# Optimization experiments

Measured on AMD Instinct MI355X. Metric: run time of the kernel, lower is better.

Reference implementation:

```python
import jax, jax.numpy as jnp
import numpy as np

B, S, N = 16, 64, 4096
D = 64            # input_dim*seq_len == output_dim*graph_dim
FEAT = 64
E = 32768
HEADS = (3, 3, 1)
NEG_SLOPE = 0.2   # PyG GATConv default negative_slope


def _lin_init(key, fi, fo):
    k1, k2 = jax.random.split(key)
    s = 1.0 / np.sqrt(fi)
    return (jax.random.uniform(k1, (fi, fo), jnp.float32, -s, s),
            jax.random.uniform(k2, (fo,), jnp.float32, -s, s))


def setup_inputs() -> dict:
    key = jax.random.key(0)
    ks = jax.random.split(key, 32)
    inp = {}
    inp["inputs"] = jax.random.normal(ks[0], (B, S, N, 1), jnp.float32)
    inp["edge_index"] = jax.random.randint(ks[1], (2, E), 0, N, dtype=jnp.int32)
    inp["W_seq"], inp["b_seq"] = _lin_init(ks[2], D, D)
    inp["src_embed"] = jax.random.normal(ks[3], (N, FEAT), jnp.float32) * 0.1
    inp["tgt_embed"] = jax.random.normal(ks[4], (FEAT, N), jnp.float32) * 0.1
    for i, H in enumerate(HEADS):
        s = 1.0 / np.sqrt(D)
        inp[f"Wg{i}"] = jax.random.uniform(ks[5 + 5 * i], (D, H * D), jnp.float32, -s, s)
        inp[f"asrc{i}"] = jax.random.normal(ks[6 + 5 * i], (H, D), jnp.float32) * 0.1
        inp[f"adst{i}"] = jax.random.normal(ks[7 + 5 * i], (H, D), jnp.float32) * 0.1
        inp[f"bg{i}"] = jnp.zeros((D,), jnp.float32)
        inp[f"Wl{i}"], inp[f"bl{i}"] = _lin_init(ks[8 + 5 * i], D, D)
    inp["Wo"], inp["bo"] = _lin_init(ks[25], D, D)
    return inp


def _gat(x, src, dst, W, a_src, a_dst, b):
    # PyG GATConv, concat=False (mean over heads). x: [B,N,D] -> [B,N,D]
    H, C = a_src.shape
    xp = jnp.einsum('bnd,dhc->bnhc', x, W.reshape(D, H, C))       # [B,N,H,C]
    al_s = jnp.einsum('bnhc,hc->bnh', xp, a_src)
    al_d = jnp.einsum('bnhc,hc->bnh', xp, a_dst)
    e = jax.nn.leaky_relu(al_s[:, src] + al_d[:, dst], NEG_SLOPE)  # [B,Et,H]

    def per_graph(e_b, xj_b):
        m = jax.ops.segment_max(e_b, dst, num_segments=N)          # [N,H]
        w = jnp.exp(e_b - m[dst])
        z = jax.ops.segment_sum(w, dst, num_segments=N)
        alpha = w / z[dst]                                         # softmax per dst node
        return jax.ops.segment_sum(xj_b * alpha[..., None], dst, num_segments=N)

    out = jax.vmap(per_graph)(e, xp[:, src])                       # [B,N,H,C]
    return out.mean(axis=2) + b


def _forward(inputs, edge_index, W_seq, b_seq, src_embed, tgt_embed,
             Wg0, asrc0, adst0, bg0, Wl0, bl0,
             Wg1, asrc1, adst1, bg1, Wl1, bl1,
             Wg2, asrc2, adst2, bg2, Wl2, bl2, Wo, bo):
    loop = jnp.arange(N, dtype=edge_index.dtype)
    src = jnp.concatenate([edge_index[0], loop])   # PyG add_self_loops=True
    dst = jnp.concatenate([edge_index[1], loop])
    h = inputs.transpose(0, 2, 3, 1).reshape(B * N, D)
    h = h @ W_seq + b_seq + h                       # seq_linear residual
    A = jax.nn.softmax(jax.nn.relu(src_embed @ tgt_embed), axis=1)  # learned adjacency [N,N]
    gat_p = [(Wg0, asrc0, adst0, bg0), (Wg1, asrc1, adst1, bg1), (Wg2, asrc2, adst2, bg2)]
    lin_p = [(Wl0, bl0), (Wl1, bl1), (Wl2, bl2)]
    for i in range(3):
        hb = h.reshape(B, N, D)
        # layer-0 GAT output is computed but unused in the original code (dead); skip it
        h_cur = _gat(hb, src, dst, *gat_p[i]).reshape(B * N, D) if i > 0 else None
        adp = jnp.einsum('mn,bnd->bmd', A, hb)      # adaptive-graph matmul (dropout in eval = identity)
        adp = (adp @ lin_p[i][0] + lin_p[i][1]).reshape(B * N, D)
        g = jax.nn.sigmoid(adp)
        if i == 0:
            origin = h @ Wo + bo
            h = jnp.tanh(h) * g + origin * (1.0 - g)
        elif i == 1:
            h = jax.nn.leaky_relu(h_cur, 0.01) * g + h * (1.0 - g)
        else:
            h = jax.nn.relu(h_cur) * g + h * (1.0 - g)
    return h.reshape(B, N, 1, D)   # [batch, node_num, output_dim, graph_dim]


def reference(inputs, edge_index, W_seq, b_seq, src_embed, tgt_embed,
              Wg0, asrc0, adst0, bg0, Wl0, bl0,
              Wg1, asrc1, adst1, bg1, Wl1, bl1,
              Wg2, asrc2, adst2, bg2, Wl2, bl2, Wo, bo):
    return _forward(inputs, edge_index, W_seq, b_seq, src_embed, tgt_embed,
                    Wg0, asrc0, adst0, bg0, Wl0, bl0,
                    Wg1, asrc1, adst1, bg1, Wl1, bl1,
                    Wg2, asrc2, adst2, bg2, Wl2, bl2, Wo, bo)
```

## Files before the change

### kernel.cpp

```cpp
#include <hip/hip_runtime.h>
#include <stdint.h>

#define NB 16
#define NN 4096
#define DD 64
#define EE 32768
#define ETOT 36864
#define ROWS 65536
#define KSPLIT 2

typedef _Float16 f16;
typedef f16   half8 __attribute__((ext_vector_type(8)));
typedef f16   f16x8 __attribute__((ext_vector_type(8)));
typedef f16   f16x4 __attribute__((ext_vector_type(4)));
typedef float f32x4 __attribute__((ext_vector_type(4)));

__device__ __forceinline__ void gload16(const f16* g, f16* l) {
  __builtin_amdgcn_global_load_lds((const __attribute__((address_space(1))) void*)g,
                                   (__attribute__((address_space(3))) void*)l, 16, 0, 0);
}

__global__ __launch_bounds__(256) void k_zero2(int* a, int* b) {
  int i = blockIdx.x * 256 + threadIdx.x;
  if (i < NN) a[i] = 0;
  else if (i < 2 * NN) b[i - NN] = 0;
}

__global__ __launch_bounds__(256) void k_count(const int* __restrict__ ei, int* __restrict__ cnt) {
  int t = blockIdx.x * 256 + threadIdx.x;
  if (t >= ETOT) return;
  int d = (t < EE) ? ei[EE + t] : (t - EE);
  atomicAdd(&cnt[d], 1);
}

__global__ __launch_bounds__(256) void k_scan(const int* __restrict__ cnt, int* __restrict__ offs) {
  __shared__ int part[256];
  int t = threadIdx.x;
  int loc[16]; int s = 0;
  #pragma unroll
  for (int i = 0; i < 16; ++i) { int v = cnt[(t << 4) + i]; loc[i] = s; s += v; }
  part[t] = s;
  __syncthreads();
  int own = s;
  for (int d = 1; d < 256; d <<= 1) {
    int u = (t >= d) ? part[t - d] : 0;
    __syncthreads();
    part[t] += u;
    __syncthreads();
  }
  int base = part[t] - own;
  #pragma unroll
  for (int i = 0; i < 16; ++i) offs[(t << 4) + i] = base + loc[i];
}

__global__ __launch_bounds__(256) void k_fill(const int* __restrict__ ei, const int* __restrict__ offs,
                                              int* __restrict__ cur, int* __restrict__ esrc,
                                              int* __restrict__ edst) {
  int t = blockIdx.x * 256 + threadIdx.x;
  if (t >= ETOT) return;
  int s, d;
  if (t < EE) { s = ei[t]; d = ei[EE + t]; } else { s = d = t - EE; }
  int p = atomicAdd(&cur[d], 1);
  esrc[offs[d] + p] = s;
  edst[offs[d] + p] = d;
}

__global__ __launch_bounds__(256) void k_seq(const float* __restrict__ inp, const float* __restrict__ Wseq,
                                             const float* __restrict__ bseq, float* __restrict__ h) {
  __shared__ float X[64 * 68];
  int t = threadIdx.x;
  int b = blockIdx.x >> 6, n0 = (blockIdx.x & 63) << 6;
  #pragma unroll
  for (int i = 0; i < 16; ++i) {
    int idx = t + (i << 8);
    int s = idx >> 6, nl = idx & 63;
    X[nl * 68 + s] = inp[((size_t)((b << 6) + s) << 12) + n0 + nl];
  }
  __syncthreads();
  int c = t & 63, rg = t >> 6;
  float Wc[64];
  #pragma unroll
  for (int k = 0; k < 64; ++k) Wc[k] = Wseq[(k << 6) + c];
  float bc = bseq[c];
  for (int rr = 0; rr < 16; ++rr) {
    int r = (rg << 4) + rr;
    float a = bc + X[r * 68 + c];
    #pragma unroll
    for (int k4 = 0; k4 < 16; ++k4) {
      float4 x = *(const float4*)&X[r * 68 + (k4 << 2)];
      a = fmaf(x.x, Wc[4*k4+0], a); a = fmaf(x.y, Wc[4*k4+1], a);
      a = fmaf(x.z, Wc[4*k4+2], a); a = fmaf(x.w, Wc[4*k4+3], a);
    }
    h[((size_t)(b << 12) + n0 + r) * 64 + c] = a;
  }
}

__global__ __launch_bounds__(256) void k_adjmm(const f16* __restrict__ SEh, const f16* __restrict__ TEh,
                                               f16* __restrict__ A, float* __restrict__ Zpart) {
  __shared__ f16 Al[2][128 * 32];
  __shared__ f16 Bl[2][128 * 32];
  const int t = threadIdx.x, lane = t & 63, w = t >> 6;
  const int m0 = blockIdx.y << 7, j0 = blockIdx.x << 7;
  const int l15 = lane & 15, lhi = lane >> 4;
  const int wm = (w >> 1) << 6, wj = (w & 1) << 6;
  f32x4 acc[4][4] = {};
  const int c0 = (w << 6) + lane;
  const int row0 = c0 >> 2, ko0 = (c0 & 3) << 3;
  const int c1 = c0 + 256;
  const int row1 = c1 >> 2, ko1 = (c1 & 3) << 3;
  const f16* ga0 = SEh + (size_t)(m0 + row0) * 64 + ko0;
  const f16* ga1 = SEh + (size_t)(m0 + row1) * 64 + ko1;
  const f16* gb0 = TEh + (size_t)(j0 + row0) * 64 + ko0;
  const f16* gb1 = TEh + (size_t)(j0 + row1) * 64 + ko1;
  #pragma unroll
  for (int kt = 0; kt < 2; ++kt) {
    const int kof = kt << 5;
    gload16(ga0 + kof, Al[kt] + c0 * 8);
    gload16(ga1 + kof, Al[kt] + c1 * 8);
    gload16(gb0 + kof, Bl[kt] + c0 * 8);
    gload16(gb1 + kof, Bl[kt] + c1 * 8);
  }
  __syncthreads();
  #pragma unroll
  for (int kt = 0; kt < 2; ++kt) {
    half8 af[4], bf[4];
    #pragma unroll
    for (int i = 0; i < 4; ++i) {
      af[i] = *(const half8*)(Al[kt] + (wm + i * 16 + l15) * 32 + lhi * 8);
      bf[i] = *(const half8*)(Bl[kt] + (wj + i * 16 + l15) * 32 + lhi * 8);
    }
    #pragma unroll
    for (int mi = 0; mi < 4; ++mi)
      #pragma unroll
      for (int nj = 0; nj < 4; ++nj)
        acc[mi][nj] = __builtin_amdgcn_mfma_f32_16x16x32_f16(af[mi], bf[nj], acc[mi][nj], 0, 0, 0);
  }
  float rs[4][4];
  #pragma unroll
  for (int mi = 0; mi < 4; ++mi)
    #pragma unroll
    for (int r = 0; r < 4; ++r) rs[mi][r] = 0.f;
  #pragma unroll
  for (int mi = 0; mi < 4; ++mi)
    #pragma unroll
    for (int nj = 0; nj < 4; ++nj)
      #pragma unroll
      for (int r = 0; r < 4; ++r) {
        int row = m0 + wm + mi * 16 + lhi * 4 + r;
        int col = j0 + wj + nj * 16 + l15;
        float e = __expf(fmaxf(acc[mi][nj][r], 0.f));
        f16 eh = (f16)e;
        A[((size_t)row << 12) + col] = eh;
        rs[mi][r] += (float)eh;
      }
  #pragma unroll
  for (int mi = 0; mi < 4; ++mi)
    #pragma unroll
    for (int r = 0; r < 4; ++r) {
      float s = rs[mi][r];
      s += __shfl_xor(s, 1); s += __shfl_xor(s, 2);
      s += __shfl_xor(s, 4); s += __shfl_xor(s, 8);
      rs[mi][r] = s;
    }
  if (l15 == 0) {
    int p = (blockIdx.x << 1) + (w & 1);
    #pragma unroll
    for (int mi = 0; mi < 4; ++mi)
      #pragma unroll
      for (int r = 0; r < 4; ++r)
        Zpart[((size_t)p << 12) + m0 + wm + mi * 16 + lhi * 4 + r] = rs[mi][r];
  }
}

__global__ __launch_bounds__(256) void k_rowz(const float* __restrict__ Zpart, float* __restrict__ rowZ) {
  int row = blockIdx.x * 256 + threadIdx.x;
  float s = 0.f;
  #pragma unroll 8
  for (int p = 0; p < 64; ++p) s += Zpart[((size_t)p << 12) + row];
  rowZ[row] = 1.f / s;
}

#define NKT 32
__global__ __launch_bounds__(512) void k_gemm8(const f16* __restrict__ A, const f16* __restrict__ BT,
                                               f16* __restrict__ Cout) {
  extern __shared__ f16 smem[];
  const int t = threadIdx.x, lane = t & 63, wid = t >> 6;
  const int wr = wid >> 1, wc = wid & 1;
  const int l15 = lane & 15, lhi = lane >> 4;
  const int h7 = l15 & 7;
  const int wgid = blockIdx.x;
  const int nid = (wgid & 7) * 32 + (wgid >> 3);
  const int z = nid >> 7, rem = nid & 127;
  const int m0 = (rem >> 3) << 8;
  const int j0 = (rem & 7) << 7;
  const size_t kbase = (size_t)z << 11;
  f16* __restrict__ Cz = Cout + ((size_t)z << 22);

  const f16* gA[4]; int lA[4];
  #pragma unroll
  for (int i = 0; i < 4; ++i) {
    int s = t + (i << 9), row = s >> 3, sl = (s & 7) ^ (row & 7);
    gA[i] = A + (size_t)(m0 + row) * 4096 + kbase + sl * 8;
    lA[i] = s * 8;
  }
  const f16* gB[2]; int lB[2];
  #pragma unroll
  for (int i = 0; i < 2; ++i) {
    int s = t + (i << 9), row = s >> 3, sl = (s & 7) ^ (row & 7);
    gB[i] = BT + (size_t)(j0 + row) * 4096 + kbase + sl * 8;
    lB[i] = 16384 + s * 8;
  }
  #define SA(buf, kt, i) gload16(gA[i] + (kt) * 64, smem + (buf) * 24576 + lA[i])
  #define SB(buf, kt, i) gload16(gB[i] + (kt) * 64, smem + (buf) * 24576 + lB[i])

  const int rbase = wr << 6;
  const int cbase = wc << 6;
  f32x4 acc[4][4] = {};

  #pragma unroll
  for (int i = 0; i < 4; ++i) SA(0, 0, i);
  #pragma unroll
  for (int i = 0; i < 2; ++i) SB(0, 0, i);
  #pragma unroll
  for (int i = 0; i < 4; ++i) SA(1, 1, i);
  #pragma unroll
  for (int i = 0; i < 2; ++i) SB(1, 1, i);
  asm volatile("s_waitcnt vmcnt(6)" ::: "memory");
  __builtin_amdgcn_sched_barrier(0);
  __builtin_amdgcn_s_barrier();
  __builtin_amdgcn_sched_barrier(0);

  int b0 = 0, b1 = 1, b2 = 2;
  for (int kt = 0; kt < NKT; ++kt) {
    const f16* Ab = smem + b0 * 24576;
    const f16* Bb = Ab + 16384;
    const bool pf = (kt + 2 < NKT);
    {
      half8 af[4], bf[4];
      #pragma unroll
      for (int mi = 0; mi < 4; ++mi) {
        int row = rbase + mi * 16 + l15;
        af[mi] = *(const half8*)(Ab + row * 64 + (lhi ^ h7) * 8);
      }
      #pragma unroll
      for (int nj = 0; nj < 4; ++nj) {
        int row = cbase + nj * 16 + l15;
        bf[nj] = *(const half8*)(Bb + row * 64 + (lhi ^ h7) * 8);
      }
      if (pf) { SA(b2, kt + 2, 0); SA(b2, kt + 2, 1); SA(b2, kt + 2, 2); }
      __builtin_amdgcn_s_setprio(1);
      #pragma unroll
      for (int mi = 0; mi < 4; ++mi)
        #pragma unroll
        for (int nj = 0; nj < 4; ++nj)
          acc[mi][nj] = __builtin_amdgcn_mfma_f32_16x16x32_f16(af[mi], bf[nj], acc[mi][nj], 0, 0, 0);
      __builtin_amdgcn_s_setprio(0);
    }
    __builtin_amdgcn_s_barrier();
    __builtin_amdgcn_sched_barrier(0);
    {
      half8 af[4], bf[4];
      #pragma unroll
      for (int mi = 0; mi < 4; ++mi) {
        int row = rbase + mi * 16 + l15;
        af[mi] = *(const half8*)(Ab + row * 64 + ((4 + lhi) ^ h7) * 8);
      }
      #pragma unroll
      for (int nj = 0; nj < 4; ++nj) {
        int row = cbase + nj * 16 + l15;
        bf[nj] = *(const half8*)(Bb + row * 64 + ((4 + lhi) ^ h7) * 8);
      }
      if (pf) { SA(b2, kt + 2, 3); SB(b2, kt + 2, 0); SB(b2, kt + 2, 1); }
      __builtin_amdgcn_s_setprio(1);
      #pragma unroll
      for (int mi = 0; mi < 4; ++mi)
        #pragma unroll
        for (int nj = 0; nj < 4; ++nj)
          acc[mi][nj] = __builtin_amdgcn_mfma_f32_16x16x32_f16(af[mi], bf[nj], acc[mi][nj], 0, 0, 0);
      __builtin_amdgcn_s_setprio(0);
    }
    if (kt < NKT - 2)       asm volatile("s_waitcnt vmcnt(6)" ::: "memory");
    else if (kt == NKT - 2) asm volatile("s_waitcnt vmcnt(0)" ::: "memory");
    __builtin_amdgcn_sched_barrier(0);
    __builtin_amdgcn_s_barrier();
    __builtin_amdgcn_sched_barrier(0);
    int tb = b0; b0 = b1; b1 = b2; b2 = tb;
  }
  #undef SA
  #undef SB
  #pragma unroll
  for (int mi = 0; mi < 4; ++mi)
    #pragma unroll
    for (int nj = 0; nj < 4; ++nj)
      #pragma unroll
      for (int r = 0; r < 4; ++r) {
        int row = m0 + rbase + mi * 16 + (lhi << 2) + r;
        int col = j0 + cbase + nj * 16 + l15;
        Cz[(size_t)row * 1024 + col] = (f16)acc[mi][nj][r];
      }
}

template<int H, int NP>
__device__ __forceinline__ void wprep_body(const float* __restrict__ Wg, const float* __restrict__ asrc,
                                           const float* __restrict__ adst, const float* __restrict__ Wl,
                                           f16* __restrict__ Wgh, int bid, int t) {
  const int WL0 = H * 64 + 16;
  for (int i = bid * 256 + t; i < NP * 64; i += 16 * 256) {
    int j = i >> 6, k = i & 63;
    float v;
    if (j < H * 64) {
      v = Wg[(size_t)k * (H * 64) + j];
    } else if (j < H * 64 + 2 * H) {
      int cc = j - H * 64, hh = cc >> 1;
      const float* a = ((cc & 1) ? adst : asrc) + (hh << 6);
      const float* wrow = Wg + (size_t)k * (H * 64) + (hh << 6);
      float s = 0.f;
      #pragma unroll 16
      for (int c = 0; c < 64; ++c) s = fmaf(wrow[c], a[c], s);
      v = s;
    } else if (j >= WL0 && j < WL0 + 64) {
      v = Wl[(k << 6) + (j - WL0)];
    } else v = 0.f;
    Wgh[(size_t)j * 64 + k] = (f16)v;
  }
}

__global__ __launch_bounds__(256) void k_allprep(
    const float* __restrict__ Wg1, const float* __restrict__ as1, const float* __restrict__ ad1,
    const float* __restrict__ Wl1, f16* __restrict__ Wgh1,
    const float* __restrict__ Wg2, const float* __restrict__ as2, const float* __restrict__ ad2,
    const float* __restrict__ Wl2, f16* __restrict__ Wgh2,
    const float* __restrict__ Wl0, const float* __restrict__ Wo, f16* __restrict__ W0h,
    const float* __restrict__ SE, const float* __restrict__ TE,
    f16* __restrict__ SEh, f16* __restrict__ TEh) {
  __shared__ float X[64 * 65];
  int bid = blockIdx.x, t = threadIdx.x;
  if (bid < 16) { wprep_body<3, 272>(Wg1, as1, ad1, Wl1, Wgh1, bid, t); return; }
  if (bid < 32) { wprep_body<1, 144>(Wg2, as2, ad2, Wl2, Wgh2, bid - 16, t); return; }
  if (bid < 40) {
    for (int i = (bid - 32) * 256 + t; i < 128 * 64; i += 8 * 256) {
      int j = i >> 6, k = i & 63;
      float v = (j < 64) ? Wl0[(k << 6) + j] : Wo[(k << 6) + (j - 64)];
      W0h[(size_t)j * 64 + k] = (f16)v;
    }
    return;
  }
  if (bid < 296) {
    int i = ((bid - 40) * 256 + t) * 4;
    float4 v = *(const float4*)(SE + i);
    f16 o[4] = {(f16)v.x, (f16)v.y, (f16)v.z, (f16)v.w};
    *(uint64_t*)(SEh + i) = *(uint64_t*)o;
    return;
  }
  int j0 = (bid - 296) << 6;
  #pragma unroll
  for (int i = 0; i < 16; ++i) {
    int idx = t + (i << 8);
    int k = idx >> 6, jl = idx & 63;
    X[jl * 65 + k] = TE[((size_t)k << 12) + j0 + jl];
  }
  __syncthreads();
  int jl = t >> 2, kg = t & 3;
  f16 o[16];
  #pragma unroll
  for (int i = 0; i < 16; ++i) o[i] = (f16)X[jl * 65 + (kg << 4) + i];
  f16* dst = TEh + ((size_t)(j0 + jl) << 6) + (kg << 4);
  *(uint64_t*)(dst + 0) = *(uint64_t*)(o + 0);
  *(uint64_t*)(dst + 4) = *(uint64_t*)(o + 4);
  *(uint64_t*)(dst + 8) = *(uint64_t*)(o + 8);
  *(uint64_t*)(dst + 12) = *(uint64_t*)(o + 12);
}

template<int H, int NP>
__global__ __launch_bounds__(256) void k_xpmm(const float* __restrict__ h, const f16* __restrict__ Wgh,
                                              f16* __restrict__ xp, float* __restrict__ als,
                                              float* __restrict__ ald, f16* __restrict__ HWlT) {
  const int WL0 = H * 64 + 16, JW0 = WL0 / 16, NT = NP / 16;
  __shared__ f16 Ah[64 * 72];
  __shared__ f16 Bh[NP * 72];
  __shared__ f16 stage[64 * 72];
  const int t = threadIdx.x, lane = t & 63, w = t >> 6;
  const size_t r0 = (size_t)blockIdx.x * 64;
  const int b = (int)(r0 >> 12), n0 = (int)(r0 & 4095);
  #pragma unroll
  for (int i = 0; i < 4; ++i) {
    int idx = t + (i << 8);
    int row = idx >> 4, k4 = (idx & 15) << 2;
    float4 v = *(const float4*)&h[(r0 + row) * 64 + k4];
    f16 o[4] = {(f16)v.x, (f16)v.y, (f16)v.z, (f16)v.w};
    *(uint64_t*)&Ah[row * 72 + k4] = *(uint64_t*)o;
  }
  for (int i = t; i < NP * 16; i += 256) {
    int row = i >> 4, k4 = (i & 15) << 2;
    *(uint64_t*)&Bh[row * 72 + k4] = *(const uint64_t*)&Wgh[(size_t)row * 64 + k4];
  }
  __syncthreads();
  const int l15 = lane & 15, lhi = lane >> 4;
  f32x4 acc[NT] = {};
  #pragma unroll
  for (int kk = 0; kk < 2; ++kk) {
    half8 af = *(const half8*)&Ah[(w * 16 + l15) * 72 + kk * 32 + lhi * 8];
    #pragma unroll
    for (int j = 0; j < NT; ++j) {
      half8 bf = *(const half8*)&Bh[(j * 16 + l15) * 72 + kk * 32 + lhi * 8];
      acc[j] = __builtin_amdgcn_mfma_f32_16x16x32_f16(af, bf, acc[j], 0, 0, 0);
    }
  }
  const int rl = w * 16 + lhi * 4;
  #pragma unroll
  for (int j = 0; j < NT; ++j) {
    int col = j * 16 + l15;
    if (j * 16 + 15 < H * 64) {
      #pragma unroll
      for (int r = 0; r < 4; ++r) {
        if (H == 3) xp[(r0 + rl + r) * 256 + ((col & 63) << 2) + (col >> 6)] = (f16)acc[j][r];
        else        xp[(r0 + rl + r) * 64 + col] = (f16)acc[j][r];
      }
    } else if (j < JW0) {
      int cc = col - H * 64;
      if (cc >= 0 && cc < 2 * H) {
        int hh = cc >> 1;
        #pragma unroll
        for (int r = 0; r < 4; ++r) {
          if (cc & 1) ald[(r0 + rl + r) * H + hh] = acc[j][r];
          else        als[(r0 + rl + r) * H + hh] = acc[j][r];
        }
      }
    } else {
      int e = col - WL0;
      f16 o[4] = {(f16)acc[j][0], (f16)acc[j][1], (f16)acc[j][2], (f16)acc[j][3]};
      *(uint64_t*)&stage[e * 72 + rl] = *(uint64_t*)o;
    }
  }
  __syncthreads();
  {
    int e = t >> 2, seg = (t & 3) << 4;
    float4 v0 = *(const float4*)&stage[e * 72 + seg];
    float4 v1 = *(const float4*)&stage[e * 72 + seg + 8];
    f16* dst = HWlT + (((size_t)((b << 6) + e)) << 12) + n0 + seg;
    *(float4*)dst = v0;
    *(float4*)(dst + 8) = v1;
  }
}

__global__ __launch_bounds__(256) void k_prep0(const float* __restrict__ h, const f16* __restrict__ W0h,
                                               f16* __restrict__ HWlT, f16* __restrict__ orig) {
  __shared__ f16 Ah[64 * 72];
  __shared__ f16 Bh[128 * 72];
  __shared__ f16 stage[64 * 72];
  const int t = threadIdx.x, lane = t & 63, w = t >> 6;
  const size_t r0 = (size_t)blockIdx.x * 64;
  const int b = (int)(r0 >> 12), n0 = (int)(r0 & 4095);
  #pragma unroll
  for (int i = 0; i < 4; ++i) {
    int idx = t + (i << 8);
    int row = idx >> 4, k4 = (idx & 15) << 2;
    float4 v = *(const float4*)&h[(r0 + row) * 64 + k4];
    f16 o[4] = {(f16)v.x, (f16)v.y, (f16)v.z, (f16)v.w};
    *(uint64_t*)&Ah[row * 72 + k4] = *(uint64_t*)o;
  }
  for (int i = t; i < 128 * 16; i += 256) {
    int row = i >> 4, k4 = (i & 15) << 2;
    *(uint64_t*)&Bh[row * 72 + k4] = *(const uint64_t*)&W0h[(size_t)row * 64 + k4];
  }
  __syncthreads();
  const int l15 = lane & 15, lhi = lane >> 4;
  f32x4 acc[8] = {};
  #pragma unroll
  for (int kk = 0; kk < 2; ++kk) {
    half8 af = *(const half8*)&Ah[(w * 16 + l15) * 72 + kk * 32 + lhi * 8];
    #pragma unroll
    for (int j = 0; j < 8; ++j) {
      half8 bf = *(const half8*)&Bh[(j * 16 + l15) * 72 + kk * 32 + lhi * 8];
      acc[j] = __builtin_amdgcn_mfma_f32_16x16x32_f16(af, bf, acc[j], 0, 0, 0);
    }
  }
  const int rl = w * 16 + lhi * 4;
  #pragma unroll
  for (int j = 0; j < 8; ++j) {
    int col = j * 16 + l15;
    if (j < 4) {
      f16 o[4] = {(f16)acc[j][0], (f16)acc[j][1], (f16)acc[j][2], (f16)acc[j][3]};
      *(uint64_t*)&stage[col * 72 + rl] = *(uint64_t*)o;
    } else {
      #pragma unroll
      for (int r = 0; r < 4; ++r)
        orig[(r0 + rl + r) * 64 + (col - 64)] = (f16)acc[j][r];
    }
  }
  __syncthreads();
  {
    int e = t >> 2, seg = (t & 3) << 4;
    float4 v0 = *(const float4*)&stage[e * 72 + seg];
    float4 v1 = *(const float4*)&stage[e * 72 + seg + 8];
    f16* dst = HWlT + (((size_t)((b << 6) + e)) << 12) + n0 + seg;
    *(float4*)dst = v0;
    *(float4*)(dst + 8) = v1;
  }
}

template<int H>
__global__ __launch_bounds__(256) void k_maxals(const float* __restrict__ als, float* __restrict__ Mals) {
  __shared__ float red[256];
  int b = blockIdx.x, t = threadIdx.x;
  size_t rbase = (size_t)b << 12;
  for (int h = 0; h < H; ++h) {
    float m = -1e30f;
    for (int n = t; n < NN; n += 256) m = fmaxf(m, als[(rbase + n) * H + h]);
    red[t] = m;
    __syncthreads();
    for (int d = 128; d; d >>= 1) {
      if (t < d) red[t] = fmaxf(red[t], red[t + d]);
      __syncthreads();
    }
    if (t == 0) Mals[b * H + h] = red[0];
    __syncthreads();
  }
}

template<int H>
__global__ __launch_bounds__(256) void k_wts(const float* __restrict__ als, const float* __restrict__ ald,
                                             const float* __restrict__ Mals, const int* __restrict__ esrc,
                                             const int* __restrict__ edst, float* __restrict__ wts) {
  const int WST = (H == 3) ? 4 : 1;
  int t = threadIdx.x, lane = t & 63, w = t >> 6;
  int gw = blockIdx.x * 4 + w;
  int b = gw & 15;
  int p = ((gw >> 4) << 6) + lane;
  size_t rbase = (size_t)b << 12;
  int s = esrc[p], n = edst[p];
  float* dst = wts + ((size_t)b * ETOT + p) * WST;
  #pragma unroll
  for (int h = 0; h < H; ++h) {
    float ad = ald[(rbase + n) * H + h];
    float B = Mals[b * H + h] + ad;
    float T = B > 0.f ? B : 0.2f * B;
    float ev = als[(rbase + s) * H + h] + ad;
    ev = ev > 0.f ? ev : 0.2f * ev;
    dst[h] = __expf(ev - T);
  }
}

template<int H, int ACT>
__global__ __launch_bounds__(256) void k_aggc(const f16* __restrict__ xp, const float* __restrict__ wts,
                                              const int* __restrict__ offs, const int* __restrict__ cnt,
                                              const int* __restrict__ esrc, const float* __restrict__ bg,
                                              const float* __restrict__ h, const f16* __restrict__ gp,
                                              const float* __restrict__ rowZ, const float* __restrict__ bl,
                                              float* __restrict__ hout) {
  const int WST = (H == 3) ? 4 : 1;
  __shared__ float wbuf[4][64 * WST];
  __shared__ int   sbuf[4][64];
  int t = threadIdx.x, lane = t & 63, wv = t >> 6;
  int blk = blockIdx.x;
  int b = ((blk & 7) << 1) | ((blk >> 3) & 1);
  int n = ((blk >> 4) << 2) + wv;
  size_t rbase = (size_t)b << 12;
  int o = offs[n], c = cnt[n];
  const float* wsrc = wts + ((size_t)b * ETOT + o) * WST;
  float z[H], acc[H];
  #pragma unroll
  for (int hh = 0; hh < H; ++hh) { z[hh] = 0.f; acc[hh] = 0.f; }
  for (int e0 = 0; e0 < c; e0 += 64) {
    int ce = min(64, c - e0);
    if (lane < ce) {
      sbuf[wv][lane] = esrc[o + e0 + lane];
      if (H == 3) *(float4*)&wbuf[wv][lane * 4] = *(const float4*)&wsrc[(size_t)(e0 + lane) * 4];
      else        wbuf[wv][lane] = wsrc[e0 + lane];
    }
    #pragma unroll 4
    for (int e = 0; e < ce; ++e) {
      int s = sbuf[wv][e];
      if (H == 3) {
        float4 w4 = *(const float4*)&wbuf[wv][e * 4];
        f16x4 q = *(const f16x4*)(xp + (((size_t)(rbase + s)) << 8) + (lane << 2));
        z[0] += w4.x; acc[0] = fmaf(w4.x, (float)q[0], acc[0]);
        z[1] += w4.y; acc[1] = fmaf(w4.y, (float)q[1], acc[1]);
        z[2] += w4.z; acc[2] = fmaf(w4.z, (float)q[2], acc[2]);
      } else {
        float wv_ = wbuf[wv][e];
        float xv = (float)xp[(((size_t)(rbase + s)) << 6) + lane];
        z[0] += wv_; acc[0] = fmaf(wv_, xv, acc[0]);
      }
    }
  }
  float r = 0.f;
  #pragma unroll
  for (int hh = 0; hh < H; ++hh) r += acc[hh] / z[hh];
  float cv = r * (1.f / H) + bg[lane];
  size_t ga = ((size_t)n << 10) + (b << 6) + lane;
  float zi = rowZ[n];
  float g0 = (float)gp[ga], g1 = (float)gp[ga + (size_t)(4096 * 1024)];
  float g = 1.f / (1.f + __expf(-((g0 + g1) * zi + bl[lane])));
  size_t ridx = ((rbase + n) << 6) + lane;
  float hv = h[ridx];
  float act = ACT ? fmaxf(cv, 0.f) : (cv > 0.f ? cv : 0.01f * cv);
  hout[ridx] = act * g + hv * (1.f - g);
}

__global__ __launch_bounds__(256) void k_comb0e(const float* __restrict__ h, const f16* __restrict__ gp,
                                                const float* __restrict__ rowZ, const f16* __restrict__ orig,
                                                const float* __restrict__ bl, const float* __restrict__ bo,
                                                float* __restrict__ hout) {
  for (size_t i4 = (size_t)blockIdx.x * 256 + threadIdx.x; i4 < (size_t)ROWS * 16; i4 += (size_t)2048 * 256) {
    size_t i = i4 * 4;
    int d = (int)(i & 63), n = (int)((i >> 6) & 4095), b = (int)(i >> 18);
    size_t ga = ((size_t)n << 10) + (b << 6) + d;
    float zi = rowZ[n];
    f16x4 g0 = *(const f16x4*)&gp[ga];
    f16x4 g1 = *(const f16x4*)&gp[ga + (size_t)(4096 * 1024)];
    f16x4 og = *(const f16x4*)&orig[i];
    float4 hv = *(const float4*)&h[i];
    float4 o;
    float* op = &o.x;
    const float* hp = &hv.x;
    #pragma unroll
    for (int r = 0; r < 4; ++r) {
      float g = 1.f / (1.f + __expf(-(((float)g0[r] + (float)g1[r]) * zi + bl[d + r])));
      float orv = (float)og[r] + bo[d + r];
      op[r] = tanhf(hp[r]) * g + orv * (1.f - g);
    }
    *(float4*)&hout[i] = o;
  }
}

extern "C" void kernel_launch(void* const* d_in, const int* in_sizes, int n_in,
                              void* d_out, int out_size, void* d_ws, size_t ws_size,
                              hipStream_t stream) {
  (void)in_sizes; (void)n_in; (void)out_size; (void)ws_size;
  const float* inp  = (const float*)d_in[0];
  const int*   ei   = (const int*)d_in[1];
  const float* Wseq = (const float*)d_in[2];
  const float* bseq = (const float*)d_in[3];
  const float* SE   = (const float*)d_in[4];
  const float* TE   = (const float*)d_in[5];
  const float* Wg[3]   = {(const float*)d_in[6],  (const float*)d_in[12], (const float*)d_in[18]};
  const float* asrc[3] = {(const float*)d_in[7],  (const float*)d_in[13], (const float*)d_in[19]};
  const float* adst[3] = {(const float*)d_in[8],  (const float*)d_in[14], (const float*)d_in[20]};
  const float* bgp[3]  = {(const float*)d_in[9],  (const float*)d_in[15], (const float*)d_in[21]};
  const float* Wl[3]   = {(const float*)d_in[10], (const float*)d_in[16], (const float*)d_in[22]};
  const float* bl[3]   = {(const float*)d_in[11], (const float*)d_in[17], (const float*)d_in[23]};
  const float* Wo = (const float*)d_in[24];
  const float* bo = (const float*)d_in[25];
  float* out = (float*)d_out;

  uint8_t* ws = (uint8_t*)d_ws;
  size_t o = 0;
  auto nxt = [&](size_t sz) { void* p = ws + o; o += (sz + 255) & ~(size_t)255; return p; };
  f16*   Af   = (f16*)  nxt((size_t)NN * NN * sizeof(f16));
  f16*   HWlT = (f16*)  nxt((size_t)1024 * NN * sizeof(f16));
  float* h    = (float*)nxt((size_t)ROWS * 64 * 4);
  f16*   gp   = (f16*)  nxt((size_t)KSPLIT * NN * 1024 * sizeof(f16));
  f16*   xp   = (f16*)  nxt((size_t)ROWS * 256 * sizeof(f16));
  f16*   orig = (f16*)  nxt((size_t)ROWS * 64 * sizeof(f16));
  float* als  = (float*)nxt((size_t)ROWS * 3 * 4);
  float* ald  = (float*)nxt((size_t)ROWS * 3 * 4);
  float* rowZ = (float*)nxt((size_t)NN * 4);
  float* Zpart= (float*)nxt((size_t)64 * NN * 4);
  f16*   SEh  = (f16*)  nxt((size_t)NN * 64 * sizeof(f16));
  f16*   TEh  = (f16*)  nxt((size_t)NN * 64 * sizeof(f16));
  f16*   Wgh1 = (f16*)  nxt((size_t)288 * 64 * sizeof(f16));
  f16*   Wgh2 = (f16*)  nxt((size_t)144 * 64 * sizeof(f16));
  f16*   W0h  = (f16*)  nxt((size_t)128 * 64 * sizeof(f16));
  float* wts  = (float*)nxt((size_t)NB * ETOT * 4 * 4);
  float* Mals = (float*)nxt((size_t)NB * 3 * 4);
  int*   cnt  = (int*)  nxt((size_t)NN * 4);
  int*   curp = (int*)  nxt((size_t)NN * 4);
  int*   offs = (int*)  nxt((size_t)NN * 4);
  int*   esrc = (int*)  nxt((size_t)ETOT * 4);
  int*   edst = (int*)  nxt((size_t)ETOT * 4);

  static bool attr_set = false;
  if (!attr_set) {
    hipFuncSetAttribute((const void*)k_gemm8, hipFuncAttributeMaxDynamicSharedMemorySize, 147456);
    attr_set = true;
  }

  dim3 blk(256);
  k_zero2<<<32, blk, 0, stream>>>(cnt, curp);
  k_count<<<144, blk, 0, stream>>>(ei, cnt);
  k_scan<<<1, blk, 0, stream>>>(cnt, offs);
  k_fill<<<144, blk, 0, stream>>>(ei, offs, curp, esrc, edst);
  k_allprep<<<360, blk, 0, stream>>>(Wg[1], asrc[1], adst[1], Wl[1], Wgh1,
                                     Wg[2], asrc[2], adst[2], Wl[2], Wgh2,
                                     Wl[0], Wo, W0h, SE, TE, SEh, TEh);
  k_seq<<<1024, blk, 0, stream>>>(inp, Wseq, bseq, h);
  k_adjmm<<<dim3(32, 32), blk, 0, stream>>>(SEh, TEh, Af, Zpart);
  k_rowz<<<16, blk, 0, stream>>>(Zpart, rowZ);
  k_prep0<<<1024, blk, 0, stream>>>(h, W0h, HWlT, orig);
  k_gemm8<<<256, 512, 147456, stream>>>(Af, HWlT, gp);
  k_comb0e<<<2048, blk, 0, stream>>>(h, gp, rowZ, orig, bl[0], bo, h);
  k_xpmm<3, 272><<<1024, blk, 0, stream>>>(h, Wgh1, xp, als, ald, HWlT);
  k_maxals<3><<<16, blk, 0, stream>>>(als, Mals);
  k_wts<3><<<2304, blk, 0, stream>>>(als, ald, Mals, esrc, edst, wts);
  k_gemm8<<<256, 512, 147456, stream>>>(Af, HWlT, gp);
  k_aggc<3, 0><<<16384, blk, 0, stream>>>(xp, wts, offs, cnt, esrc, bgp[1], h, gp, rowZ, bl[1], h);
  k_xpmm<1, 144><<<1024, blk, 0, stream>>>(h, Wgh2, xp, als, ald, HWlT);
  k_maxals<1><<<16, blk, 0, stream>>>(als, Mals);
  k_wts<1><<<2304, blk, 0, stream>>>(als, ald, Mals, esrc, edst, wts);
  k_gemm8<<<256, 512, 147456, stream>>>(Af, HWlT, gp);
  k_aggc<1, 1><<<16384, blk, 0, stream>>>(xp, wts, offs, cnt, esrc, bgp[2], h, gp, rowZ, bl[2], out);
}
```

Baseline: 301.9 us.

## Widen adjacency GEMM tiles to 256x256 with four-way K split and double buffering

The adjacency GEMM kernel now uses 256x256 output tiles, with 8 waves laid out 2x4 and 8x4 MFMA accumulators per wave. The K dimension is split four ways instead of two, and the three-stage LDS ring is replaced by a two-stage double buffer that waits on vmcnt(0) each iteration. The combine kernels are updated to sum KSPLIT partial results. The goal is more MFMA work per LDS byte loaded and less shared memory per block. The cost is twice the partial-sum write and read traffic, less load/compute overlap, and higher register pressure.

After: 302.0 us. Within noise of the previous version (+0.0%).

```diff
diff --git a/kernel.cpp b/kernel.cpp
--- a/kernel.cpp
+++ b/kernel.cpp
@@ -7,7 +7,7 @@
 #define EE 32768
 #define ETOT 36864
 #define ROWS 65536
-#define KSPLIT 2
+#define KSPLIT 4
 
 typedef _Float16 f16;
 typedef f16   half8 __attribute__((ext_vector_type(8)));
@@ -180,20 +180,20 @@
   rowZ[row] = 1.f / s;
 }
 
-#define NKT 32
+#define NKT 16
 __global__ __launch_bounds__(512) void k_gemm8(const f16* __restrict__ A, const f16* __restrict__ BT,
                                                f16* __restrict__ Cout) {
   extern __shared__ f16 smem[];
   const int t = threadIdx.x, lane = t & 63, wid = t >> 6;
-  const int wr = wid >> 1, wc = wid & 1;
+  const int wr = wid >> 2, wc = wid & 3;
   const int l15 = lane & 15, lhi = lane >> 4;
   const int h7 = l15 & 7;
   const int wgid = blockIdx.x;
   const int nid = (wgid & 7) * 32 + (wgid >> 3);
-  const int z = nid >> 7, rem = nid & 127;
-  const int m0 = (rem >> 3) << 8;
-  const int j0 = (rem & 7) << 7;
-  const size_t kbase = (size_t)z << 11;
+  const int z = nid >> 6, rem = nid & 63;
+  const int m0 = (rem >> 2) << 8;
+  const int j0 = (rem & 3) << 8;
+  const size_t kbase = (size_t)z << 10;
   f16* __restrict__ Cz = Cout + ((size_t)z << 22);
 
   const f16* gA[4]; int lA[4];
@@ -203,42 +203,38 @@
     gA[i] = A + (size_t)(m0 + row) * 4096 + kbase + sl * 8;
     lA[i] = s * 8;
   }
-  const f16* gB[2]; int lB[2];
-  #pragma unroll
-  for (int i = 0; i < 2; ++i) {
+  const f16* gB[4]; int lB[4];
+  #pragma unroll
+  for (int i = 0; i < 4; ++i) {
     int s = t + (i << 9), row = s >> 3, sl = (s & 7) ^ (row & 7);
     gB[i] = BT + (size_t)(j0 + row) * 4096 + kbase + sl * 8;
     lB[i] = 16384 + s * 8;
   }
-  #define SA(buf, kt, i) gload16(gA[i] + (kt) * 64, smem + (buf) * 24576 + lA[i])
-  #define SB(buf, kt, i) gload16(gB[i] + (kt) * 64, smem + (buf) * 24576 + lB[i])
-
-  const int rbase = wr << 6;
+  #define SA(buf, kt, i) gload16(gA[i] + (kt) * 64, smem + (buf) * 32768 + lA[i])
+  #define SB(buf, kt, i) gload16(gB[i] + (kt) * 64, smem + (buf) * 32768 + lB[i])
+
+  const int rbase = wr << 7;
   const int cbase = wc << 6;
-  f32x4 acc[4][4] = {};
+  f32x4 acc[8][4] = {};
 
   #pragma unroll
   for (int i = 0; i < 4; ++i) SA(0, 0, i);
   #pragma unroll
-  for (int i = 0; i < 2; ++i) SB(0, 0, i);
-  #pragma unroll
-  for (int i = 0; i < 4; ++i) SA(1, 1, i);
-  #pragma unroll
-  for (int i = 0; i < 2; ++i) SB(1, 1, i);
-  asm volatile("s_waitcnt vmcnt(6)" ::: "memory");
+  for (int i = 0; i < 4; ++i) SB(0, 0, i);
+  asm volatile("s_waitcnt vmcnt(0)" ::: "memory");
   __builtin_amdgcn_sched_barrier(0);
   __builtin_amdgcn_s_barrier();
   __builtin_amdgcn_sched_barrier(0);
 
-  int b0 = 0, b1 = 1, b2 = 2;
   for (int kt = 0; kt < NKT; ++kt) {
-    const f16* Ab = smem + b0 * 24576;
+    const int cur = kt & 1;
+    const f16* Ab = smem + cur * 32768;
     const f16* Bb = Ab + 16384;
-    const bool pf = (kt + 2 < NKT);
+    const bool pf = (kt + 1 < NKT);
     {
-      half8 af[4], bf[4];
-      #pragma unroll
-      for (int mi = 0; mi < 4; ++mi) {
+      half8 af[8], bf[4];
+      #pragma unroll
+      for (int mi = 0; mi < 8; ++mi) {
         int row = rbase + mi * 16 + l15;
         af[mi] = *(const half8*)(Ab + row * 64 + (lhi ^ h7) * 8);
       }
@@ -247,21 +243,19 @@
         int row = cbase + nj * 16 + l15;
         bf[nj] = *(const half8*)(Bb + row * 64 + (lhi ^ h7) * 8);
       }
-      if (pf) { SA(b2, kt + 2, 0); SA(b2, kt + 2, 1); SA(b2, kt + 2, 2); }
+      if (pf) { SA(cur ^ 1, kt + 1, 0); SA(cur ^ 1, kt + 1, 1); SA(cur ^ 1, kt + 1, 2); SA(cur ^ 1, kt + 1, 3); }
       __builtin_amdgcn_s_setprio(1);
       #pragma unroll
-      for (int mi = 0; mi < 4; ++mi)
+      for (int mi = 0; mi < 8; ++mi)
         #pragma unroll
         for (int nj = 0; nj < 4; ++nj)
           acc[mi][nj] = __builtin_amdgcn_mfma_f32_16x16x32_f16(af[mi], bf[nj], acc[mi][nj], 0, 0, 0);
       __builtin_amdgcn_s_setprio(0);
     }
-    __builtin_amdgcn_s_barrier();
-    __builtin_amdgcn_sched_barrier(0);
     {
-      half8 af[4], bf[4];
-      #pragma unroll
-      for (int mi = 0; mi < 4; ++mi) {
+      half8 af[8], bf[4];
+      #pragma unroll
+      for (int mi = 0; mi < 8; ++mi) {
         int row = rbase + mi * 16 + l15;
         af[mi] = *(const half8*)(Ab + row * 64 + ((4 + lhi) ^ h7) * 8);
       }
@@ -270,26 +264,26 @@
         int row = cbase + nj * 16 + l15;
         bf[nj] = *(const half8*)(Bb + row * 64 + ((4 + lhi) ^ h7) * 8);
       }
-      if (pf) { SA(b2, kt + 2, 3); SB(b2, kt + 2, 0); SB(b2, kt + 2, 1); }
+      if (pf) { SB(cur ^ 1, kt + 1, 0); SB(cur ^ 1, kt + 1, 1); SB(cur ^ 1, kt + 1, 2); SB(cur ^ 1, kt + 1, 3); }
       __builtin_amdgcn_s_setprio(1);
       #pragma unroll
-      for (int mi = 0; mi < 4; ++mi)
+      for (int mi = 0; mi < 8; ++mi)
         #pragma unroll
         for (int nj = 0; nj < 4; ++nj)
           acc[mi][nj] = __builtin_amdgcn_mfma_f32_16x16x32_f16(af[mi], bf[nj], acc[mi][nj], 0, 0, 0);
       __builtin_amdgcn_s_setprio(0);
     }
-    if (kt < NKT - 2)       asm volatile("s_waitcnt vmcnt(6)" ::: "memory");
-    else if (kt == NKT - 2) asm volatile("s_waitcnt vmcnt(0)" ::: "memory");
-    __builtin_amdgcn_sched_barrier(0);
-    __builtin_amdgcn_s_barrier();
-    __builtin_amdgcn_sched_barrier(0);
-    int tb = b0; b0 = b1; b1 = b2; b2 = tb;
+    if (pf) {
+      asm volatile("s_waitcnt vmcnt(0)" ::: "memory");
+      __builtin_amdgcn_sched_barrier(0);
+      __builtin_amdgcn_s_barrier();
+      __builtin_amdgcn_sched_barrier(0);
+    }
   }
   #undef SA
   #undef SB
   #pragma unroll
-  for (int mi = 0; mi < 4; ++mi)
+  for (int mi = 0; mi < 8; ++mi)
     #pragma unroll
     for (int nj = 0; nj < 4; ++nj)
       #pragma unroll
@@ -590,8 +584,10 @@
   float cv = r * (1.f / H) + bg[lane];
   size_t ga = ((size_t)n << 10) + (b << 6) + lane;
   float zi = rowZ[n];
-  float g0 = (float)gp[ga], g1 = (float)gp[ga + (size_t)(4096 * 1024)];
-  float g = 1.f / (1.f + __expf(-((g0 + g1) * zi + bl[lane])));
+  float gs = 0.f;
+  #pragma unroll
+  for (int p = 0; p < KSPLIT; ++p) gs += (float)gp[ga + (size_t)p * (4096 * 1024)];
+  float g = 1.f / (1.f + __expf(-(gs * zi + bl[lane])));
   size_t ridx = ((rbase + n) << 6) + lane;
   float hv = h[ridx];
   float act = ACT ? fmaxf(cv, 0.f) : (cv > 0.f ? cv : 0.01f * cv);
@@ -607,8 +603,12 @@
     int d = (int)(i & 63), n = (int)((i >> 6) & 4095), b = (int)(i >> 18);
     size_t ga = ((size_t)n << 10) + (b << 6) + d;
     float zi = rowZ[n];
-    f16x4 g0 = *(const f16x4*)&gp[ga];
-    f16x4 g1 = *(const f16x4*)&gp[ga + (size_t)(4096 * 1024)];
+    float gs[4] = {0.f, 0.f, 0.f, 0.f};
+    #pragma unroll
+    for (int p = 0; p < KSPLIT; ++p) {
+      f16x4 gq = *(const f16x4*)&gp[ga + (size_t)p * (4096 * 1024)];
+      gs[0] += (float)gq[0]; gs[1] += (float)gq[1]; gs[2] += (float)gq[2]; gs[3] += (float)gq[3];
+    }
     f16x4 og = *(const f16x4*)&orig[i];
     float4 hv = *(const float4*)&h[i];
     float4 o;
@@ -616,7 +616,7 @@
     const float* hp = &hv.x;
     #pragma unroll
     for (int r = 0; r < 4; ++r) {
-      float g = 1.f / (1.f + __expf(-(((float)g0[r] + (float)g1[r]) * zi + bl[d + r])));
+      float g = 1.f / (1.f + __expf(-(gs[r] * zi + bl[d + r])));
       float orv = (float)og[r] + bo[d + r];
       op[r] = tanhf(hp[r]) * g + orv * (1.f - g);
     }
@@ -672,7 +672,7 @@
 
   static bool attr_set = false;
   if (!attr_set) {
-    hipFuncSetAttribute((const void*)k_gemm8, hipFuncAttributeMaxDynamicSharedMemorySize, 147456);
+    hipFuncSetAttribute((const void*)k_gemm8, hipFuncAttributeMaxDynamicSharedMemorySize, 131072);
     attr_set = true;
   }
 
@@ -688,16 +688,16 @@
   k_adjmm<<<dim3(32, 32), blk, 0, stream>>>(SEh, TEh, Af, Zpart);
   k_rowz<<<16, blk, 0, stream>>>(Zpart, rowZ);
   k_prep0<<<1024, blk, 0, stream>>>(h, W0h, HWlT, orig);
-  k_gemm8<<<256, 512, 147456, stream>>>(Af, HWlT, gp);
+  k_gemm8<<<256, 512, 131072, stream>>>(Af, HWlT, gp);
   k_comb0e<<<2048, blk, 0, stream>>>(h, gp, rowZ, orig, bl[0], bo, h);
   k_xpmm<3, 272><<<1024, blk, 0, stream>>>(h, Wgh1, xp, als, ald, HWlT);
   k_maxals<3><<<16, blk, 0, stream>>>(als, Mals);
   k_wts<3><<<2304, blk, 0, stream>>>(als, ald, Mals, esrc, edst, wts);
-  k_gemm8<<<256, 512, 147456, stream>>>(Af, HWlT, gp);
+  k_gemm8<<<256, 512, 131072, stream>>>(Af, HWlT, gp);
   k_aggc<3, 0><<<16384, blk, 0, stream>>>(xp, wts, offs, cnt, esrc, bgp[1], h, gp, rowZ, bl[1], h);
   k_xpmm<1, 144><<<1024, blk, 0, stream>>>(h, Wgh2, xp, als, ald, HWlT);
   k_maxals<1><<<16, blk, 0, stream>>>(als, Mals);
   k_wts<1><<<2304, blk, 0, stream>>>(als, ald, Mals, esrc, edst, wts);
-  k_gemm8<<<256, 512, 147456, stream>>>(Af, HWlT, gp);
+  k_gemm8<<<256, 512, 131072, stream>>>(Af, HWlT, gp);
   k_aggc<1, 1><<<16384, blk, 0, stream>>>(xp, wts, offs, cnt, esrc, bgp[2], h, gp, rowZ, bl[2], out);
 }
```
